# Performance work log

Measured on AMD Instinct MI355X. Metric: run time of the kernel, lower is better.

Reference implementation:

```python
import jax, jax.numpy as jnp
import numpy as np
from jax import lax

WINDOW_SIZE = 11
SIGMA = 1.5
RGB_RANGE = 1.0
K1, K2 = 0.01, 0.03
CHANNELS = 3


def gaussian_window(window_size, sigma, channels, dtype=jnp.float32):
    coords = jnp.arange(window_size, dtype=dtype) - window_size // 2
    g = jnp.exp(-(coords ** 2) / (2.0 * sigma * sigma))
    g = g / g.sum()
    w2d = jnp.outer(g, g)
    w2d = w2d / w2d.sum()
    # depthwise kernel: (C, 1, ws, ws) in OIHW with feature_group_count=C
    return jnp.broadcast_to(w2d, (channels, 1, window_size, window_size)).astype(dtype)


def _dwconv(inp, window, padding):
    # depthwise conv2d, groups = C
    C = inp.shape[1]
    return lax.conv_general_dilated(
        inp, window,
        window_strides=(1, 1),
        padding=[(padding, padding), (padding, padding)],
        feature_group_count=C,
        dimension_numbers=('NCHW', 'OIHW', 'NCHW'))


def setup_inputs() -> dict:
    key = jax.random.key(0)
    kx, ky = jax.random.split(key)
    B, C, H, W = 16, CHANNELS, 512, 512
    x = jax.random.uniform(kx, (B, C, H, W), dtype=jnp.float32)
    y = jax.random.uniform(ky, (B, C, H, W), dtype=jnp.float32)
    window = gaussian_window(WINDOW_SIZE, SIGMA, C)
    return {"x": x, "y": y, "window": window}


def reference(x, y, window):
    padding = WINDOW_SIZE // 2
    mu_x = _dwconv(x, window, padding)
    mu_y = _dwconv(y, window, padding)
    mu_x2 = mu_x * mu_x
    mu_y2 = mu_y * mu_y
    mu_xy = mu_x * mu_y
    sigma_x2 = _dwconv(x * x, window, padding) - mu_x2
    sigma_y2 = _dwconv(y * y, window, padding) - mu_y2
    sigma_xy = _dwconv(x * y, window, padding) - mu_xy
    L = RGB_RANGE
    C1 = (K1 * L) ** 2
    C2 = (K2 * L) ** 2
    ssim_map = ((2.0 * mu_xy + C1) * (2.0 * sigma_xy + C2)) / (
        (mu_x2 + mu_y2 + C1) * (sigma_x2 + sigma_y2 + C2) + 1e-12)
    loss = 1.0 - ssim_map
    return loss.mean()
```

## Files before the change

### kernel.cpp

```cpp
#include <hip/hip_runtime.h>


typedef __fp16 f16x8 __attribute__((ext_vector_type(8)));
typedef __fp16 f16x4 __attribute__((ext_vector_type(4)));
typedef float  f32x4 __attribute__((ext_vector_type(4)));
typedef unsigned u32x2 __attribute__((ext_vector_type(2)));
typedef unsigned u32x4 __attribute__((ext_vector_type(4)));

__device__ __forceinline__ unsigned pk2(float a, float b) {
    return __builtin_bit_cast(unsigned, __builtin_amdgcn_cvt_pkrtz(a, b));
}
__device__ __forceinline__ f32x4 mfmaB(f16x8 a, f16x8 b, f32x4 c) {
    return __builtin_amdgcn_mfma_f32_16x16x32_f16(a, b, c, 0, 0, 0);
}
__device__ __forceinline__ f32x4 mfmaC(f16x4 a, f16x4 b, f32x4 c) {
    return __builtin_amdgcn_mfma_f32_16x16x16f16(a, b, c, 0, 0, 0);
}

__global__ __launch_bounds__(256, 6) void ssim_main(
    const float* __restrict__ xg, const float* __restrict__ yg,
    const float* __restrict__ w2d, float* __restrict__ part)
{
    __shared__ float gsf[11];
    __shared__ unsigned tbp[64];
    __shared__ float wred[4];

    const int tid = threadIdx.x;

    if (tid < 11) {
        float s = 0.0f;
        #pragma unroll
        for (int j = 0; j < 11; ++j) s += w2d[tid * 11 + j];
        gsf[tid] = s;
    }
    __syncthreads();

    if (tid < 64) {
        float ssum = 0.0f;
        #pragma unroll
        for (int k = 0; k < 11; ++k)
            if (k != 5) ssum += (float)(__fp16)gsf[k];
        const __fp16 cc = (__fp16)(1.0f - ssum);
        auto tap = [&](int t) -> __fp16 {
            if ((unsigned)t > 10u) return (__fp16)0.f;
            return (t == 5) ? cc : (__fp16)gsf[t];
        };
        const int t = tid - 19;
        const unsigned short lo = __builtin_bit_cast(unsigned short, tap(t));
        const unsigned short hi = __builtin_bit_cast(unsigned short, tap(t + 1));
        tbp[tid] = (unsigned)lo | ((unsigned)hi << 16);
    }
    __syncthreads();

    const int lane = tid & 63, wv = tid >> 6;
    const int lm = lane & 15, lg = lane >> 4;

    const int nblk = (int)gridDim.x;
    const int bid = (int)blockIdx.x;
    const int swz = (bid & 7) * (nblk >> 3) + (bid >> 3);
    const int t = swz * 4 + wv;
    const int tz = t >> 10, ty = (t >> 5) & 31, tx = t & 31;
    const int x0 = 16 * tx - 8, y0 = 16 * ty - 8;
    const bool border = (tx == 0) | (tx == 31) | (ty == 0) | (ty == 31);
    const float* __restrict__ xp = xg + (size_t)tz * (512 * 512);
    const float* __restrict__ yp = yg + (size_t)tz * (512 * 512);

    auto ldband = [&](const float* __restrict__ p, int b) -> f16x8 {
        const int gr = y0 + 16 * b + lm;
        const int gc0 = x0 + 8 * lg;
        u32x4 w;
        if (!border) {
            const float4 v0 = *(const float4*)&p[gr * 512 + gc0];
            const float4 v1 = *(const float4*)&p[gr * 512 + gc0 + 4];
            w = (u32x4){pk2(v0.x, v0.y), pk2(v0.z, v0.w),
                        pk2(v1.x, v1.y), pk2(v1.z, v1.w)};
        } else {
            const bool rok = (unsigned)gr < 512u;
            float v[8];
            #pragma unroll
            for (int j = 0; j < 8; ++j) {
                const int gc = gc0 + j;
                const bool ok = rok & ((unsigned)gc < 512u);
                const int o = ok ? (gr * 512 + gc) : 0;
                v[j] = ok ? p[o] : 0.f;
            }
            w = (u32x4){pk2(v[0], v[1]), pk2(v[2], v[3]),
                        pk2(v[4], v[5]), pk2(v[6], v[7])};
        }
        return __builtin_bit_cast(f16x8, w);
    };

    const f16x8 xd0 = ldband(xp, 0), xd1 = ldband(xp, 1);
    const f16x8 yd0 = ldband(yp, 0), yd1 = ldband(yp, 1);

    f16x8 bt;
    f16x4 ca0, ca1;
    {
        const int ib = 8 * lg - lm + 16;
        const u32x4 wb = {tbp[ib], tbp[ib + 2], tbp[ib + 4], tbp[ib + 6]};
        bt = __builtin_bit_cast(f16x8, wb);
        const int ic = 4 * lg - lm + 16;
        const u32x2 w0 = {tbp[ic], tbp[ic + 2]};
        const u32x2 w1 = {tbp[ic + 16], tbp[ic + 18]};
        ca0 = __builtin_bit_cast(f16x4, w0);
        ca1 = __builtin_bit_cast(f16x4, w1);
    }

    const f32x4 z4 = {0.f, 0.f, 0.f, 0.f};
    f32x4 acc[5];
    #pragma unroll
    for (int q = 0; q < 5; ++q) {
        f16x8 a0, a1;
        if (q == 0)      { a0 = xd0;       a1 = xd1; }
        else if (q == 1) { a0 = yd0;       a1 = yd1; }
        else if (q == 2) { a0 = xd0 * xd0; a1 = xd1 * xd1; }
        else if (q == 3) { a0 = yd0 * yd0; a1 = yd1 * yd1; }
        else             { a0 = xd0 * yd0; a1 = xd1 * yd1; }
        const f32x4 d0 = mfmaB(a0, bt, z4);
        const f32x4 d1 = mfmaB(a1, bt, z4);
        const u32x2 h0 = {pk2(d0[0], d0[1]), pk2(d0[2], d0[3])};
        const u32x2 h1 = {pk2(d1[0], d1[1]), pk2(d1[2], d1[3])};
        const f32x4 p0 = mfmaC(ca0, __builtin_bit_cast(f16x4, h0), z4);
        acc[q]         = mfmaC(ca1, __builtin_bit_cast(f16x4, h1), p0);
    }

    float lsum = 0.0f;
    const float C1 = 1e-4f, C2 = 9e-4f;
    #pragma unroll
    for (int r = 0; r < 4; ++r) {
        const float mx = acc[0][r], my = acc[1][r];
        const float exx = acc[2][r], eyy = acc[3][r];
        const float exy = acc[4][r];
        const float mx2 = mx * mx, my2 = my * my, mxy = mx * my;
        const float vx = exx - mx2, vy = eyy - my2, vxy = exy - mxy;
        const float num = (2.0f * mxy + C1) * (2.0f * vxy + C2);
        const float den = (mx2 + my2 + C1) * (vx + vy + C2) + 1e-12f;
        lsum = fmaf(num, __builtin_amdgcn_rcpf(den), lsum);
    }

    #pragma unroll
    for (int off = 32; off > 0; off >>= 1)
        lsum += __shfl_down(lsum, off, 64);
    if ((tid & 63) == 0) wred[tid >> 6] = lsum;
    __syncthreads();
    if (tid == 0)
        part[bid] = wred[0] + wred[1] + wred[2] + wred[3];
}

__global__ __launch_bounds__(1024) void ssim_reduce(
    const float* __restrict__ part, float* __restrict__ out,
    int n, float invN)
{
    __shared__ float wred[16];
    float s = 0.0f;
    for (int i = threadIdx.x; i < n; i += 1024) s += part[i];
    #pragma unroll
    for (int off = 32; off > 0; off >>= 1)
        s += __shfl_down(s, off, 64);
    if ((threadIdx.x & 63) == 0) wred[threadIdx.x >> 6] = s;
    __syncthreads();
    if (threadIdx.x == 0) {
        float tot = 0.0f;
        #pragma unroll
        for (int w = 0; w < 16; ++w) tot += wred[w];
        out[0] = 1.0f - tot * invN;
    }
}

extern "C" void kernel_launch(void* const* d_in, const int* in_sizes, int n_in,
                              void* d_out, int out_size, void* d_ws, size_t ws_size,
                              hipStream_t stream) {
    const float* x   = (const float*)d_in[0];
    const float* y   = (const float*)d_in[1];
    const float* w2d = (const float*)d_in[2];
    float* out  = (float*)d_out;
    float* part = (float*)d_ws;

    const int H = 512, W = 512;
    const int total = in_sizes[0];
    const int Z = total / (H * W);

    const int nblk = Z * 1024 / 4;
    ssim_main<<<dim3(nblk), 256, 0, stream>>>(x, y, w2d, part);

    const float invN = 1.0f / (float)total;
    ssim_reduce<<<1, 1024, 0, stream>>>(part, out, nblk, invN);
}
```

Baseline: 162.3 us.

## Stage shared 48x48 halo tile in LDS for four 16x16 wave tiles

```diff
diff --git a/kernel.cpp b/kernel.cpp
--- a/kernel.cpp
+++ b/kernel.cpp
@@ -16,16 +16,60 @@
 __device__ __forceinline__ f32x4 mfmaC(f16x4 a, f16x4 b, f32x4 c) {
     return __builtin_amdgcn_mfma_f32_16x16x16f16(a, b, c, 0, 0, 0);
 }
-
-__global__ __launch_bounds__(256, 6) void ssim_main(
+__device__ __forceinline__ void ldsBarrier() {
+    asm volatile("s_waitcnt lgkmcnt(0)\n\ts_barrier" ::: "memory");
+}
+
+#define SXW 28
+
+__global__ __launch_bounds__(256, 8) void ssim_main(
     const float* __restrict__ xg, const float* __restrict__ yg,
     const float* __restrict__ w2d, float* __restrict__ part)
 {
+    __shared__ __align__(16) unsigned sx[48 * SXW];
+    __shared__ __align__(16) unsigned sy[48 * SXW];
+    __shared__ unsigned tbp[64];
     __shared__ float gsf[11];
-    __shared__ unsigned tbp[64];
     __shared__ float wred[4];
 
     const int tid = threadIdx.x;
+
+    const int nblk = (int)gridDim.x;
+    const int bid = (int)blockIdx.x;
+    const int swz = (bid & 7) * (nblk >> 3) + (bid >> 3);
+    const int tz = swz >> 8, ty = (swz >> 4) & 15, tx = swz & 15;
+    const int X0 = 32 * tx - 8, Y0 = 32 * ty - 8;
+    const bool inter = (tx > 0) & (tx < 15) & (ty > 0) & (ty < 15);
+    const float* __restrict__ xp = xg + (size_t)tz * (512 * 512);
+    const float* __restrict__ yp = yg + (size_t)tz * (512 * 512);
+
+    float4 lx0, ly0, lx1, ly1, lx2, ly2;
+    const bool h2 = tid < 64;
+    auto ldit = [&](int it, float4& vx, float4& vy) {
+        const int r = it / 12, c4 = it - r * 12;
+        const int gr = Y0 + r, gc0 = X0 + 4 * c4;
+        if (inter) {
+            const int o = gr * 512 + gc0;
+            vx = *(const float4*)&xp[o];
+            vy = *(const float4*)&yp[o];
+        } else {
+            const bool rok = (unsigned)gr < 512u;
+            float tx4[4], ty4[4];
+            #pragma unroll
+            for (int j = 0; j < 4; ++j) {
+                const int gc = gc0 + j;
+                const bool ok = rok & ((unsigned)gc < 512u);
+                const int o = ok ? (gr * 512 + gc) : 0;
+                tx4[j] = ok ? xp[o] : 0.f;
+                ty4[j] = ok ? yp[o] : 0.f;
+            }
+            vx = make_float4(tx4[0], tx4[1], tx4[2], tx4[3]);
+            vy = make_float4(ty4[0], ty4[1], ty4[2], ty4[3]);
+        }
+    };
+    ldit(tid, lx0, ly0);
+    ldit(tid + 256, lx1, ly1);
+    if (h2) ldit(tid + 512, lx2, ly2);
 
     if (tid < 11) {
         float s = 0.0f;
@@ -33,8 +77,6 @@
         for (int j = 0; j < 11; ++j) s += w2d[tid * 11 + j];
         gsf[tid] = s;
     }
-    __syncthreads();
-
     if (tid < 64) {
         float ssum = 0.0f;
         #pragma unroll
@@ -50,48 +92,22 @@
         const unsigned short hi = __builtin_bit_cast(unsigned short, tap(t + 1));
         tbp[tid] = (unsigned)lo | ((unsigned)hi << 16);
     }
-    __syncthreads();
+
+    auto wrt = [&](int it, const float4& vx, const float4& vy) {
+        const int r = it / 12, c4 = it - r * 12;
+        *(uint2*)&sx[r * SXW + 2 * c4] =
+            make_uint2(pk2(vx.x, vx.y), pk2(vx.z, vx.w));
+        *(uint2*)&sy[r * SXW + 2 * c4] =
+            make_uint2(pk2(vy.x, vy.y), pk2(vy.z, vy.w));
+    };
+    wrt(tid, lx0, ly0);
+    wrt(tid + 256, lx1, ly1);
+    if (h2) wrt(tid + 512, lx2, ly2);
+    ldsBarrier();
 
     const int lane = tid & 63, wv = tid >> 6;
     const int lm = lane & 15, lg = lane >> 4;
-
-    const int nblk = (int)gridDim.x;
-    const int bid = (int)blockIdx.x;
-    const int swz = (bid & 7) * (nblk >> 3) + (bid >> 3);
-    const int t = swz * 4 + wv;
-    const int tz = t >> 10, ty = (t >> 5) & 31, tx = t & 31;
-    const int x0 = 16 * tx - 8, y0 = 16 * ty - 8;
-    const bool border = (tx == 0) | (tx == 31) | (ty == 0) | (ty == 31);
-    const float* __restrict__ xp = xg + (size_t)tz * (512 * 512);
-    const float* __restrict__ yp = yg + (size_t)tz * (512 * 512);
-
-    auto ldband = [&](const float* __restrict__ p, int b) -> f16x8 {
-        const int gr = y0 + 16 * b + lm;
-        const int gc0 = x0 + 8 * lg;
-        u32x4 w;
-        if (!border) {
-            const float4 v0 = *(const float4*)&p[gr * 512 + gc0];
-            const float4 v1 = *(const float4*)&p[gr * 512 + gc0 + 4];
-            w = (u32x4){pk2(v0.x, v0.y), pk2(v0.z, v0.w),
-                        pk2(v1.x, v1.y), pk2(v1.z, v1.w)};
-        } else {
-            const bool rok = (unsigned)gr < 512u;
-            float v[8];
-            #pragma unroll
-            for (int j = 0; j < 8; ++j) {
-                const int gc = gc0 + j;
-                const bool ok = rok & ((unsigned)gc < 512u);
-                const int o = ok ? (gr * 512 + gc) : 0;
-                v[j] = ok ? p[o] : 0.f;
-            }
-            w = (u32x4){pk2(v[0], v[1]), pk2(v[2], v[3]),
-                        pk2(v[4], v[5]), pk2(v[6], v[7])};
-        }
-        return __builtin_bit_cast(f16x8, w);
-    };
-
-    const f16x8 xd0 = ldband(xp, 0), xd1 = ldband(xp, 1);
-    const f16x8 yd0 = ldband(yp, 0), yd1 = ldband(yp, 1);
+    const int wr = wv >> 1, wc = wv & 1;
 
     f16x8 bt;
     f16x4 ca0, ca1;
@@ -105,6 +121,12 @@
         ca0 = __builtin_bit_cast(f16x4, w0);
         ca1 = __builtin_bit_cast(f16x4, w1);
     }
+
+    const int rbase = (16 * wr + lm) * SXW + 8 * wc + 4 * lg;
+    const f16x8 xd0 = __builtin_bit_cast(f16x8, *(const u32x4*)&sx[rbase]);
+    const f16x8 xd1 = __builtin_bit_cast(f16x8, *(const u32x4*)&sx[rbase + 16 * SXW]);
+    const f16x8 yd0 = __builtin_bit_cast(f16x8, *(const u32x4*)&sy[rbase]);
+    const f16x8 yd1 = __builtin_bit_cast(f16x8, *(const u32x4*)&sy[rbase + 16 * SXW]);
 
     const f32x4 z4 = {0.f, 0.f, 0.f, 0.f};
     f32x4 acc[5];
@@ -142,7 +164,7 @@
     for (int off = 32; off > 0; off >>= 1)
         lsum += __shfl_down(lsum, off, 64);
     if ((tid & 63) == 0) wred[tid >> 6] = lsum;
-    __syncthreads();
+    ldsBarrier();
     if (tid == 0)
         part[bid] = wred[0] + wred[1] + wred[2] + wred[3];
 }
@@ -180,7 +202,7 @@
     const int total = in_sizes[0];
     const int Z = total / (H * W);
 
-    const int nblk = Z * 1024 / 4;
+    const int nblk = Z * 256;
     ssim_main<<<dim3(nblk), 256, 0, stream>>>(x, y, w2d, part);
 
     const float invN = 1.0f / (float)total;
```

Result: faster. 142.3 us (-12.3%).
